# Kernel optimization log

Hardware: AMD Instinct MI355X
Metric: run time of the kernel (lower is better)

Reference implementation:

```python
import jax, jax.numpy as jnp
import numpy as np

B, T, D = 4, 2048, 1024

def setup_inputs() -> dict:
    key = jax.random.key(0)
    kx, kq, kk, kv = jax.random.split(key, 4)
    lim = 1.0 / np.sqrt(D)
    x = jax.random.normal(kx, (B, T, D), dtype=jnp.float32)
    # nn.Linear weights (stored as [out,in]); applied as x @ W.T
    W_q = jax.random.uniform(kq, (D, D), jnp.float32, -lim, lim)
    W_k = jax.random.uniform(kk, (D, D), jnp.float32, -lim, lim)
    W_v = jax.random.uniform(kv, (D, D), jnp.float32, -lim, lim)
    return {"x": x, "W_q": W_q, "W_k": W_k, "W_v": W_v}

def reference(x, W_q, W_k, W_v):
    d = x.shape[-1]
    Q = jnp.einsum('btd,ed->bte', x, W_q)
    K = jnp.einsum('btd,ed->bte', x, W_k)
    V = jnp.einsum('btd,ed->bte', x, W_v)
    att = jnp.einsum('bqd,bkd->bqk', Q, K) / jnp.sqrt(jnp.asarray(d, x.dtype))
    weights = jax.nn.softmax(att, axis=-1)  # NOTE: original applies no causal mask
    return jnp.einsum('bqk,bkd->bqd', weights, V)
```

## Files before the change

kernel.cpp:

```cpp
#include <hip/hip_runtime.h>
#include <hip/hip_bf16.h>
#include <math.h>
#include <type_traits>


typedef short shortx8 __attribute__((ext_vector_type(8)));
typedef short shortx4 __attribute__((ext_vector_type(4)));
typedef float floatx16 __attribute__((ext_vector_type(16)));
typedef __attribute__((address_space(3))) void lds_void_t;
typedef __attribute__((address_space(1))) const void gmem_void_t;

#define GLD16(gp, lp) \
    __builtin_amdgcn_global_load_lds((gmem_void_t*)(gp), (lds_void_t*)(lp), 16, 0, 0)

#define MODE_PROJ 0
#define MODE_EXP  1
#define MODE_DIV  2

template <int MODE>
__global__ __launch_bounds__(512, 4) void mfma_gemm_abt(
    const __hip_bfloat16* __restrict__ A, const __hip_bfloat16* __restrict__ B,
    void* __restrict__ Cv, float* __restrict__ rowsum,
    __hip_bfloat16* __restrict__ Vt,
    int M, int N, int K, long sA, long sB, long sC, float alpha)
{
    __shared__ __hip_bfloat16 lds[3 * 12288];

    using CT = std::conditional_t<MODE == MODE_DIV, float, __hip_bfloat16>;

    const int z = blockIdx.z;
    A += (long)z * sA;
    B += (long)z * sB;
    CT* C = (CT*)Cv + (long)z * sC;

    const int t     = threadIdx.x;
    const int wave  = t >> 6;
    const int lane  = t & 63;
    const int m0    = blockIdx.x * 256;
    const int n0    = blockIdx.y * 128;
    const int wm    = (wave >> 1) * 64;
    const int wn    = (wave & 1) * 64;
    const int lrow  = lane & 31;
    const int lhalf = lane >> 5;

    const long KU   = (long)(K >> 4);
    const long aOff = (long)((m0 >> 5) + wave) * KU * 512 + lane * 8;
    const long bOff = ((long)((n0 >> 5) + (wave >> 1)) * KU + (wave & 1)) * 512
                      + lane * 8;
    const int  dA   = wave * 1024;
    const int  dB   = 8192 + wave * 512;

    const int raB = (wave >> 1) * 2048 + lane * 8;
    const int rbB = 8192 + (wave & 1) * 2048 + lane * 8;

#define STAGE(bo_, k2_) do {                                               \
        GLD16(A + aOff + (long)(k2_) * 512,       lds + (bo_) + dA);       \
        GLD16(A + aOff + (long)((k2_) + 1) * 512, lds + (bo_) + dA + 512); \
        GLD16(B + bOff + (long)(k2_) * 512,       lds + (bo_) + dB);       \
    } while (0)

    floatx16 acc[2][2] = {};
    const int KT = K >> 5;

    STAGE(0, 0);
    STAGE(12288, 2);

    int rCur = 0;
    int rNxt = 24576;

    for (int kt = 0; kt < KT; ++kt) {
        if (kt == KT - 1) {
            asm volatile("s_waitcnt vmcnt(0)" ::: "memory");
        } else {
            asm volatile("s_waitcnt vmcnt(3)" ::: "memory");
        }
        __builtin_amdgcn_s_barrier();
        if (kt + 2 < KT)
            STAGE(rNxt, 2 * (kt + 2));

        const __hip_bfloat16* Ls = lds + rCur;

        #pragma unroll
        for (int s = 0; s < 2; ++s) {
            shortx8 a[2], b[2];
            #pragma unroll
            for (int i = 0; i < 2; ++i)
                a[i] = *(const shortx8*)(Ls + raB + (2 * i + s) * 512);
            #pragma unroll
            for (int j = 0; j < 2; ++j)
                b[j] = *(const shortx8*)(Ls + rbB + (2 * j + s) * 512);
            __builtin_amdgcn_s_setprio(1);
            #pragma unroll
            for (int i = 0; i < 2; ++i)
                #pragma unroll
                for (int j = 0; j < 2; ++j)
                    acc[i][j] = __builtin_amdgcn_mfma_f32_32x32x16_bf16(
                        a[i], b[j], acc[i][j], 0, 0, 0);
            __builtin_amdgcn_s_setprio(0);
        }
        rCur = (rCur == 24576) ? 0 : rCur + 12288;
        rNxt = (rNxt == 24576) ? 0 : rNxt + 12288;
    }
#undef STAGE

    auto sidx = [&](int row, int col) -> long {
        return ((long)(row >> 5) * (N >> 4) + (col >> 4)) * 512
             + ((row & 31) + 32 * ((col >> 3) & 1)) * 8 + (col & 7);
    };

    if constexpr (MODE == MODE_PROJ) {
        if (z == 2) {
            const int bz   = m0 >> 11;
            const long bo  = (long)bz * N * 2048;
            #pragma unroll
            for (int i = 0; i < 2; ++i)
                #pragma unroll
                for (int j = 0; j < 2; ++j)
                    #pragma unroll
                    for (int g = 0; g < 4; ++g) {
                        const int t0 = (m0 + wm + 32 * i + g * 8 + 4 * lhalf) & 2047;
                        const int d  = n0 + wn + 32 * j + lrow;
                        shortx4 pk;
                        #pragma unroll
                        for (int r = 0; r < 4; ++r) {
                            __hip_bfloat16 hb = __float2bfloat16(acc[i][j][4 * g + r]);
                            pk[r] = *(short*)&hb;
                        }
                        const long idx = bo
                            + ((long)(d >> 5) * 128 + (t0 >> 4)) * 512
                            + ((d & 31) + 32 * ((t0 >> 3) & 1)) * 8 + (t0 & 7);
                        *(shortx4*)(Vt + idx) = pk;
                    }
        } else {
            #pragma unroll
            for (int i = 0; i < 2; ++i)
                #pragma unroll
                for (int j = 0; j < 2; ++j)
                    #pragma unroll
                    for (int g = 0; g < 4; ++g)
                        #pragma unroll
                        for (int r = 0; r < 4; ++r) {
                            const int row = m0 + wm + 32 * i + g * 8 + 4 * lhalf + r;
                            const int col = n0 + wn + 32 * j + lrow;
                            C[sidx(row, col)] = __float2bfloat16(acc[i][j][4 * g + r]);
                        }
        }
    } else if constexpr (MODE == MODE_EXP) {
        #pragma unroll
        for (int i = 0; i < 2; ++i) {
            float rs[16];
            #pragma unroll
            for (int reg = 0; reg < 16; ++reg) rs[reg] = 0.0f;
            #pragma unroll
            for (int j = 0; j < 2; ++j)
                #pragma unroll
                for (int g = 0; g < 4; ++g)
                    #pragma unroll
                    for (int r = 0; r < 4; ++r) {
                        const int row = m0 + wm + 32 * i + g * 8 + 4 * lhalf + r;
                        const int col = n0 + wn + 32 * j + lrow;
                        const float e = __expf(acc[i][j][4 * g + r] * alpha);
                        rs[4 * g + r] += e;
                        C[sidx(row, col)] = __float2bfloat16(e);
                    }
            #pragma unroll
            for (int reg = 0; reg < 16; ++reg) {
                float v = rs[reg];
                v += __shfl_xor(v, 1);
                v += __shfl_xor(v, 2);
                v += __shfl_xor(v, 4);
                v += __shfl_xor(v, 8);
                v += __shfl_xor(v, 16);
                if (lrow == 0) {
                    const long row = m0 + wm + 32 * i + (reg >> 2) * 8 + 4 * lhalf + (reg & 3);
                    atomicAdd(&rowsum[(long)z * M + row], v);
                }
            }
        }
    } else {
        #pragma unroll
        for (int i = 0; i < 2; ++i) {
            float inv[16];
            #pragma unroll
            for (int g = 0; g < 4; ++g)
                #pragma unroll
                for (int r = 0; r < 4; ++r) {
                    const long row = m0 + wm + 32 * i + g * 8 + 4 * lhalf + r;
                    inv[4 * g + r] = 1.0f / rowsum[(long)z * M + row];
                }
            #pragma unroll
            for (int j = 0; j < 2; ++j)
                #pragma unroll
                for (int g = 0; g < 4; ++g)
                    #pragma unroll
                    for (int r = 0; r < 4; ++r) {
                        const long row = m0 + wm + 32 * i + g * 8 + 4 * lhalf + r;
                        const long col = n0 + wn + 32 * j + lrow;
                        C[row * N + col] = acc[i][j][4 * g + r] * inv[4 * g + r];
                    }
        }
    }
}

__global__ __launch_bounds__(256) void prep(
    const float* __restrict__ x,
    const float* __restrict__ W0, const float* __restrict__ W1,
    const float* __restrict__ W2,
    __hip_bfloat16* __restrict__ xb, __hip_bfloat16* __restrict__ Wb,
    float* __restrict__ rowsum)
{
    __shared__ __hip_bfloat16 sb[32768];

    const int b  = blockIdx.x;
    const int tt = threadIdx.x;

    if (b < 32) {
        float4 zz; zz.x = zz.y = zz.z = zz.w = 0.0f;
        ((float4*)rowsum)[b * 256 + tt] = zz;
    }

    const float* src;
    __hip_bfloat16* dst;
    if (b < 256) {
        src = x + (long)b * 32 * 1024;
        dst = xb + (long)b * 32768;
    } else {
        const int w  = (b - 256) >> 5;
        const int rg = (b - 256) & 31;
        src = ((w == 0) ? W0 : (w == 1) ? W1 : W2) + (long)rg * 32 * 1024;
        dst = Wb + (long)w * 1048576 + (long)rg * 32768;
    }

    #pragma unroll
    for (int it = 0; it < 32; ++it) {
        const int idx4 = it * 256 + tt;
        const float4 f = ((const float4*)src)[idx4];
        const int row = idx4 >> 8;
        const int k0  = (idx4 & 255) << 2;
        const int p   = ((row & 31) + 32 * ((k0 >> 3) & 1)) * 8 + (k0 & 7);
        shortx4 pk;
        __hip_bfloat16 h0 = __float2bfloat16(f.x); pk[0] = *(short*)&h0;
        __hip_bfloat16 h1 = __float2bfloat16(f.y); pk[1] = *(short*)&h1;
        __hip_bfloat16 h2 = __float2bfloat16(f.z); pk[2] = *(short*)&h2;
        __hip_bfloat16 h3 = __float2bfloat16(f.w); pk[3] = *(short*)&h3;
        *(shortx4*)(sb + (k0 >> 4) * 512 + p) = pk;
    }
    __syncthreads();

    #pragma unroll
    for (int ot = 0; ot < 16; ++ot) {
        const int off = ot * 2048 + tt * 8;
        *(shortx8*)(dst + off) = *(const shortx8*)(sb + off);
    }
}

extern "C" void kernel_launch(void* const* d_in, const int* in_sizes, int n_in,
                              void* d_out, int out_size, void* d_ws, size_t ws_size,
                              hipStream_t stream)
{
    constexpr int  Bb = 4, T = 2048, D = 1024;
    constexpr int  M  = Bb * T;
    constexpr long TD = (long)T * D;
    constexpr long TT = (long)T * T;
    constexpr long MD = (long)M * D;

    const float* x  = (const float*)d_in[0];
    const float* Wq = (const float*)d_in[1];
    const float* Wk = (const float*)d_in[2];
    const float* Wv = (const float*)d_in[3];
    float* out = (float*)d_out;

    __hip_bfloat16* Q  = (__hip_bfloat16*)d_ws;
    __hip_bfloat16* Kb = Q + MD;
    __hip_bfloat16* Vt = Kb + MD;
    __hip_bfloat16* P  = Vt + MD;
    __hip_bfloat16* xb = P + (long)Bb * TT;
    __hip_bfloat16* Wb = xb + MD;
    float*     rowsum  = (float*)(Wb + 3L * D * D);

    prep<<<dim3(352), dim3(256), 0, stream>>>(x, Wq, Wk, Wv, xb, Wb, rowsum);

    dim3 blk(512);

    mfma_gemm_abt<MODE_PROJ><<<dim3(M / 256, D / 128, 3), blk, 0, stream>>>(
        xb, Wb, Q, nullptr, Vt, M, D, D, 0, (long)D * D, MD, 1.0f);

    mfma_gemm_abt<MODE_EXP><<<dim3(T / 256, T / 128, Bb), blk, 0, stream>>>(
        Q, Kb, P, rowsum, nullptr, T, T, D, TD, TD, TT, 0.03125f);

    mfma_gemm_abt<MODE_DIV><<<dim3(T / 256, D / 128, Bb), blk, 0, stream>>>(
        P, Vt, out, rowsum, nullptr, T, D, T, TT, TD, TD, 1.0f);

    (void)in_sizes; (void)n_in; (void)out_size; (void)ws_size;
}
```

Baseline: 245.6 us.

## Split-K the P·V GEMM into two halves with atomic accumulation

The final P·V GEMM now launches twice as many blocks, and each block handles half of the K range (the T dimension). Partial results are combined with float atomicAdd into the output, which the prep kernel now zeroes using extra blocks. The aim is better occupancy of the GPU's compute units, since the original grid had only 256 blocks. In exchange it doubles output traffic through atomics, makes the result non-deterministic in summation order, and adds a zeroing pass over the output.

```diff
diff --git a/kernel.cpp b/kernel.cpp
--- a/kernel.cpp
+++ b/kernel.cpp
@@ -28,10 +28,14 @@
 
     using CT = std::conditional_t<MODE == MODE_DIV, float, __hip_bfloat16>;
 
-    const int z = blockIdx.z;
-    A += (long)z * sA;
-    B += (long)z * sB;
-    CT* C = (CT*)Cv + (long)z * sC;
+    const int z  = blockIdx.z;
+    const int zb = (MODE == MODE_DIV) ? (z >> 1) : z;
+    A += (long)zb * sA;
+    B += (long)zb * sB;
+    CT* C = (CT*)Cv + (long)zb * sC;
+
+    const int ktS = (MODE == MODE_DIV) ? (z & 1) * (K >> 6) : 0;
+    const int ktE = ktS + ((MODE == MODE_DIV) ? (K >> 6) : (K >> 5));
 
     const int t     = threadIdx.x;
     const int wave  = t >> 6;
@@ -60,22 +64,21 @@
     } while (0)
 
     floatx16 acc[2][2] = {};
-    const int KT = K >> 5;
-
-    STAGE(0, 0);
-    STAGE(12288, 2);
+
+    STAGE(0, 2 * ktS);
+    STAGE(12288, 2 * ktS + 2);
 
     int rCur = 0;
     int rNxt = 24576;
 
-    for (int kt = 0; kt < KT; ++kt) {
-        if (kt == KT - 1) {
+    for (int kt = ktS; kt < ktE; ++kt) {
+        if (kt == ktE - 1) {
             asm volatile("s_waitcnt vmcnt(0)" ::: "memory");
         } else {
             asm volatile("s_waitcnt vmcnt(3)" ::: "memory");
         }
         __builtin_amdgcn_s_barrier();
-        if (kt + 2 < KT)
+        if (kt + 2 < ktE)
             STAGE(rNxt, 2 * (kt + 2));
 
         const __hip_bfloat16* Ls = lds + rCur;
@@ -173,7 +176,7 @@
                 v += __shfl_xor(v, 16);
                 if (lrow == 0) {
                     const long row = m0 + wm + 32 * i + (reg >> 2) * 8 + 4 * lhalf + (reg & 3);
-                    atomicAdd(&rowsum[(long)z * M + row], v);
+                    atomicAdd(&rowsum[(long)zb * M + row], v);
                 }
             }
         }
@@ -186,7 +189,7 @@
                 #pragma unroll
                 for (int r = 0; r < 4; ++r) {
                     const long row = m0 + wm + 32 * i + g * 8 + 4 * lhalf + r;
-                    inv[4 * g + r] = 1.0f / rowsum[(long)z * M + row];
+                    inv[4 * g + r] = 1.0f / rowsum[(long)zb * M + row];
                 }
             #pragma unroll
             for (int j = 0; j < 2; ++j)
@@ -196,7 +199,8 @@
                     for (int r = 0; r < 4; ++r) {
                         const long row = m0 + wm + 32 * i + g * 8 + 4 * lhalf + r;
                         const long col = n0 + wn + 32 * j + lrow;
-                        C[row * N + col] = acc[i][j][4 * g + r] * inv[4 * g + r];
+                        atomicAdd(&C[row * N + col],
+                                  acc[i][j][4 * g + r] * inv[4 * g + r]);
                     }
         }
     }
@@ -207,12 +211,21 @@
     const float* __restrict__ W0, const float* __restrict__ W1,
     const float* __restrict__ W2,
     __hip_bfloat16* __restrict__ xb, __hip_bfloat16* __restrict__ Wb,
-    float* __restrict__ rowsum)
+    float* __restrict__ rowsum, float* __restrict__ outz)
 {
     __shared__ __hip_bfloat16 sb[32768];
 
     const int b  = blockIdx.x;
     const int tt = threadIdx.x;
+
+    if (b >= 352) {
+        float4 zz; zz.x = zz.y = zz.z = zz.w = 0.0f;
+        float4* o = (float4*)outz + (long)(b - 352) * 4096;
+        #pragma unroll
+        for (int it = 0; it < 16; ++it)
+            o[it * 256 + tt] = zz;
+        return;
+    }
 
     if (b < 32) {
         float4 zz; zz.x = zz.y = zz.z = zz.w = 0.0f;
@@ -278,7 +291,7 @@
     __hip_bfloat16* Wb = xb + MD;
     float*     rowsum  = (float*)(Wb + 3L * D * D);
 
-    prep<<<dim3(352), dim3(256), 0, stream>>>(x, Wq, Wk, Wv, xb, Wb, rowsum);
+    prep<<<dim3(864), dim3(256), 0, stream>>>(x, Wq, Wk, Wv, xb, Wb, rowsum, out);
 
     dim3 blk(512);
 
@@ -288,7 +301,7 @@
     mfma_gemm_abt<MODE_EXP><<<dim3(T / 256, T / 128, Bb), blk, 0, stream>>>(
         Q, Kb, P, rowsum, nullptr, T, T, D, TD, TD, TT, 0.03125f);
 
-    mfma_gemm_abt<MODE_DIV><<<dim3(T / 256, D / 128, Bb), blk, 0, stream>>>(
+    mfma_gemm_abt<MODE_DIV><<<dim3(T / 256, D / 128, 2 * Bb), blk, 0, stream>>>(
         P, Vt, out, rowsum, nullptr, T, D, T, TT, TD, TD, 1.0f);
 
     (void)in_sizes; (void)n_in; (void)out_size; (void)ws_size;
```

Result: slower. 276.8 us (+12.7%).

## Overlap V projection with QK^T exp GEMM in a single fused launch

Applied to the files above, without the earlier changes.

The projection GEMM is split so that only Q and K are computed first. The V projection (written transposed) is then run in the same launch as the QK^T/exp/rowsum GEMM, using a block-index split, so the two independent workloads share the GPU. The shared GEMM body is factored into a device function with constant strides. This aims to fill idle compute units and cut tail effects, at the cost of uneven block durations inside the fused grid.

```diff
diff --git a/kernel.cpp b/kernel.cpp
--- a/kernel.cpp
+++ b/kernel.cpp
@@ -17,27 +17,19 @@
 #define MODE_EXP  1
 #define MODE_DIV  2
 
-template <int MODE>
-__global__ __launch_bounds__(512, 4) void mfma_gemm_abt(
+template <int MODE, bool VTP>
+__device__ __forceinline__ void gemm_core(
     const __hip_bfloat16* __restrict__ A, const __hip_bfloat16* __restrict__ B,
-    void* __restrict__ Cv, float* __restrict__ rowsum,
+    void* __restrict__ Cv, float* __restrict__ rs,
     __hip_bfloat16* __restrict__ Vt,
-    int M, int N, int K, long sA, long sB, long sC, float alpha)
-{
-    __shared__ __hip_bfloat16 lds[3 * 12288];
-
+    int N, int K, float alpha, int m0, int n0, __hip_bfloat16* lds)
+{
     using CT = std::conditional_t<MODE == MODE_DIV, float, __hip_bfloat16>;
-
-    const int z = blockIdx.z;
-    A += (long)z * sA;
-    B += (long)z * sB;
-    CT* C = (CT*)Cv + (long)z * sC;
+    CT* C = (CT*)Cv;
 
     const int t     = threadIdx.x;
     const int wave  = t >> 6;
     const int lane  = t & 63;
-    const int m0    = blockIdx.x * 256;
-    const int n0    = blockIdx.y * 128;
     const int wm    = (wave >> 1) * 64;
     const int wn    = (wave & 1) * 64;
     const int lrow  = lane & 31;
@@ -64,7 +56,6 @@
 
     STAGE(0, 0);
     STAGE(12288, 2);
-
     int rCur = 0;
     int rNxt = 24576;
 
@@ -108,49 +99,47 @@
              + ((row & 31) + 32 * ((col >> 3) & 1)) * 8 + (col & 7);
     };
 
-    if constexpr (MODE == MODE_PROJ) {
-        if (z == 2) {
-            const int bz   = m0 >> 11;
-            const long bo  = (long)bz * N * 2048;
-            #pragma unroll
-            for (int i = 0; i < 2; ++i)
-                #pragma unroll
-                for (int j = 0; j < 2; ++j)
+    if constexpr (MODE == MODE_PROJ && VTP) {
+        const int bz   = m0 >> 11;
+        const long bo2 = (long)bz * N * 2048;
+        #pragma unroll
+        for (int i = 0; i < 2; ++i)
+            #pragma unroll
+            for (int j = 0; j < 2; ++j)
+                #pragma unroll
+                for (int g = 0; g < 4; ++g) {
+                    const int t0 = (m0 + wm + 32 * i + g * 8 + 4 * lhalf) & 2047;
+                    const int d  = n0 + wn + 32 * j + lrow;
+                    shortx4 pk;
                     #pragma unroll
-                    for (int g = 0; g < 4; ++g) {
-                        const int t0 = (m0 + wm + 32 * i + g * 8 + 4 * lhalf) & 2047;
-                        const int d  = n0 + wn + 32 * j + lrow;
-                        shortx4 pk;
-                        #pragma unroll
-                        for (int r = 0; r < 4; ++r) {
-                            __hip_bfloat16 hb = __float2bfloat16(acc[i][j][4 * g + r]);
-                            pk[r] = *(short*)&hb;
-                        }
-                        const long idx = bo
-                            + ((long)(d >> 5) * 128 + (t0 >> 4)) * 512
-                            + ((d & 31) + 32 * ((t0 >> 3) & 1)) * 8 + (t0 & 7);
-                        *(shortx4*)(Vt + idx) = pk;
+                    for (int r = 0; r < 4; ++r) {
+                        __hip_bfloat16 hb = __float2bfloat16(acc[i][j][4 * g + r]);
+                        pk[r] = *(short*)&hb;
                     }
-        } else {
-            #pragma unroll
-            for (int i = 0; i < 2; ++i)
-                #pragma unroll
-                for (int j = 0; j < 2; ++j)
+                    const long idx = bo2
+                        + ((long)(d >> 5) * 128 + (t0 >> 4)) * 512
+                        + ((d & 31) + 32 * ((t0 >> 3) & 1)) * 8 + (t0 & 7);
+                    *(shortx4*)(Vt + idx) = pk;
+                }
+    } else if constexpr (MODE == MODE_PROJ) {
+        #pragma unroll
+        for (int i = 0; i < 2; ++i)
+            #pragma unroll
+            for (int j = 0; j < 2; ++j)
+                #pragma unroll
+                for (int g = 0; g < 4; ++g)
                     #pragma unroll
-                    for (int g = 0; g < 4; ++g)
-                        #pragma unroll
-                        for (int r = 0; r < 4; ++r) {
-                            const int row = m0 + wm + 32 * i + g * 8 + 4 * lhalf + r;
-                            const int col = n0 + wn + 32 * j + lrow;
-                            C[sidx(row, col)] = __float2bfloat16(acc[i][j][4 * g + r]);
-                        }
-        }
+                    for (int r = 0; r < 4; ++r) {
+                        const int row = m0 + wm + 32 * i + g * 8 + 4 * lhalf + r;
+                        const int col = n0 + wn + 32 * j + lrow;
+                        C[sidx(row, col)] = __float2bfloat16(acc[i][j][4 * g + r]);
+                    }
     } else if constexpr (MODE == MODE_EXP) {
         #pragma unroll
         for (int i = 0; i < 2; ++i) {
-            float rs[16];
-            #pragma unroll
-            for (int reg = 0; reg < 16; ++reg) rs[reg] = 0.0f;
+            float rsl[16];
+            #pragma unroll
+            for (int reg = 0; reg < 16; ++reg) rsl[reg] = 0.0f;
             #pragma unroll
             for (int j = 0; j < 2; ++j)
                 #pragma unroll
@@ -160,12 +149,12 @@
                         const int row = m0 + wm + 32 * i + g * 8 + 4 * lhalf + r;
                         const int col = n0 + wn + 32 * j + lrow;
                         const float e = __expf(acc[i][j][4 * g + r] * alpha);
-                        rs[4 * g + r] += e;
+                        rsl[4 * g + r] += e;
                         C[sidx(row, col)] = __float2bfloat16(e);
                     }
             #pragma unroll
             for (int reg = 0; reg < 16; ++reg) {
-                float v = rs[reg];
+                float v = rsl[reg];
                 v += __shfl_xor(v, 1);
                 v += __shfl_xor(v, 2);
                 v += __shfl_xor(v, 4);
@@ -173,7 +162,7 @@
                 v += __shfl_xor(v, 16);
                 if (lrow == 0) {
                     const long row = m0 + wm + 32 * i + (reg >> 2) * 8 + 4 * lhalf + (reg & 3);
-                    atomicAdd(&rowsum[(long)z * M + row], v);
+                    atomicAdd(&rs[row], v);
                 }
             }
         }
@@ -186,7 +175,7 @@
                 #pragma unroll
                 for (int r = 0; r < 4; ++r) {
                     const long row = m0 + wm + 32 * i + g * 8 + 4 * lhalf + r;
-                    inv[4 * g + r] = 1.0f / rowsum[(long)z * M + row];
+                    inv[4 * g + r] = 1.0f / rs[row];
                 }
             #pragma unroll
             for (int j = 0; j < 2; ++j)
@@ -200,6 +189,56 @@
                     }
         }
     }
+}
+
+__global__ __launch_bounds__(512, 4) void k_projqk(
+    const __hip_bfloat16* __restrict__ xb, const __hip_bfloat16* __restrict__ Wb,
+    __hip_bfloat16* __restrict__ Q)
+{
+    __shared__ __hip_bfloat16 lds[3 * 12288];
+    const int z = blockIdx.z;
+    gemm_core<MODE_PROJ, false>(
+        xb, Wb + (long)z * 1048576, Q + (long)z * 8388608, nullptr, nullptr,
+        1024, 1024, 1.0f, blockIdx.x * 256, blockIdx.y * 128, lds);
+}
+
+__global__ __launch_bounds__(512, 4) void k_fused(
+    const __hip_bfloat16* __restrict__ Q, const __hip_bfloat16* __restrict__ Kb,
+    __hip_bfloat16* __restrict__ P, float* __restrict__ rowsum,
+    const __hip_bfloat16* __restrict__ xb, const __hip_bfloat16* __restrict__ WbV,
+    __hip_bfloat16* __restrict__ Vt)
+{
+    __shared__ __hip_bfloat16 lds[3 * 12288];
+    const int bid = blockIdx.x;
+    if (bid < 512) {
+        const int zb = bid >> 7;
+        const int r  = bid & 127;
+        const int m0 = (r & 7) * 256;
+        const int n0 = (r >> 3) * 128;
+        gemm_core<MODE_EXP, false>(
+            Q  + (long)zb * 2097152, Kb + (long)zb * 2097152,
+            P  + (long)zb * 4194304, rowsum + (long)zb * 2048, nullptr,
+            2048, 1024, 0.03125f, m0, n0, lds);
+    } else {
+        const int p  = bid - 512;
+        const int m0 = (p & 31) * 256;
+        const int n0 = (p >> 5) * 128;
+        gemm_core<MODE_PROJ, true>(
+            xb, WbV, nullptr, nullptr, Vt,
+            1024, 1024, 1.0f, m0, n0, lds);
+    }
+}
+
+__global__ __launch_bounds__(512, 4) void k_div(
+    const __hip_bfloat16* __restrict__ P, const __hip_bfloat16* __restrict__ Vt,
+    float* __restrict__ out, float* __restrict__ rowsum)
+{
+    __shared__ __hip_bfloat16 lds[3 * 12288];
+    const int z = blockIdx.z;
+    gemm_core<MODE_DIV, false>(
+        P + (long)z * 4194304, Vt + (long)z * 2097152,
+        out + (long)z * 2097152, rowsum + (long)z * 2048, nullptr,
+        1024, 2048, 1.0f, blockIdx.x * 256, blockIdx.y * 128, lds);
 }
 
 __global__ __launch_bounds__(256) void prep(
@@ -260,7 +299,6 @@
 {
     constexpr int  Bb = 4, T = 2048, D = 1024;
     constexpr int  M  = Bb * T;
-    constexpr long TD = (long)T * D;
     constexpr long TT = (long)T * T;
     constexpr long MD = (long)M * D;
 
@@ -280,16 +318,13 @@
 
     prep<<<dim3(352), dim3(256), 0, stream>>>(x, Wq, Wk, Wv, xb, Wb, rowsum);
 
-    dim3 blk(512);
-
-    mfma_gemm_abt<MODE_PROJ><<<dim3(M / 256, D / 128, 3), blk, 0, stream>>>(
-        xb, Wb, Q, nullptr, Vt, M, D, D, 0, (long)D * D, MD, 1.0f);
-
-    mfma_gemm_abt<MODE_EXP><<<dim3(T / 256, T / 128, Bb), blk, 0, stream>>>(
-        Q, Kb, P, rowsum, nullptr, T, T, D, TD, TD, TT, 0.03125f);
-
-    mfma_gemm_abt<MODE_DIV><<<dim3(T / 256, D / 128, Bb), blk, 0, stream>>>(
-        P, Vt, out, rowsum, nullptr, T, D, T, TT, TD, TD, 1.0f);
+    k_projqk<<<dim3(M / 256, D / 128, 2), dim3(512), 0, stream>>>(xb, Wb, Q);
+
+    k_fused<<<dim3(768), dim3(512), 0, stream>>>(
+        Q, Kb, P, rowsum, xb, Wb + 2L * D * D, Vt);
+
+    k_div<<<dim3(T / 256, D / 128, Bb), dim3(512), 0, stream>>>(
+        P, Vt, out, rowsum);
 
     (void)in_sizes; (void)n_in; (void)out_size; (void)ws_size;
 }
```

Result: faster. 239.6 us (-2.4%).
